# Performance work log

Hardware: AMD Instinct MI355X
Metric: run time of the kernel (lower is better)

The kernel has to match this reference:

```python
import jax, jax.numpy as jnp
import numpy as np

N, E, D = 100000, 1600000, 64
L = 3          # num_layers
EPS = 1e-5     # LayerNorm eps


def setup_inputs() -> dict:
    key = jax.random.key(0)
    ks = jax.random.split(key, 8)
    s = 0.05
    return {
        "x": jax.random.normal(ks[0], (N, D), jnp.float32),
        "edge_src": jax.random.randint(ks[1], (E,), 0, N, jnp.int32),
        "edge_dst": jax.random.randint(ks[2], (E,), 0, N, jnp.int32),
        # SAGEConv: lin_l (on aggregated neighbors, with bias), lin_r (root, no bias)
        "w_l": (jax.random.normal(ks[3], (L, D, D)) * s).astype(jnp.float32),
        "b_l": jnp.zeros((L, D), jnp.float32),
        "w_r": (jax.random.normal(ks[4], (L, D, D)) * s).astype(jnp.float32),
        # LayerNorm affine params per layer
        "gamma": jnp.ones((L, D), jnp.float32),
        "beta": jnp.zeros((L, D), jnp.float32),
        # residual projection (layer 0 only; Identity afterwards)
        "w_res": (jax.random.normal(ks[5], (D, D)) * s).astype(jnp.float32),
        "b_res": jnp.zeros((D,), jnp.float32),
        # final fc
        "w_fc": (jax.random.normal(ks[6], (D, D)) * s).astype(jnp.float32),
        "b_fc": jnp.zeros((D,), jnp.float32),
    }


def _layer_norm(h, g, b):
    mu = jnp.mean(h, axis=-1, keepdims=True)
    var = jnp.var(h, axis=-1, keepdims=True)
    return (h - mu) * jax.lax.rsqrt(var + EPS) * g + b


def reference(x, edge_src, edge_dst, w_l, b_l, w_r, gamma, beta, w_res, b_res, w_fc, b_fc):
    n = x.shape[0]
    # in-degree for mean aggregation (nodes with no in-edges get 0 aggregate)
    deg = jax.ops.segment_sum(jnp.ones(edge_dst.shape, x.dtype), edge_dst, num_segments=n)
    inv_deg = jnp.where(deg > 0, 1.0 / jnp.maximum(deg, 1.0), 0.0)[:, None]  # [N,1]
    for i in range(L):
        residual = x @ w_res + b_res if i == 0 else x
        # SAGEConv mean aggregation: gather source feats, scatter-sum at dst, divide by degree
        agg = jax.ops.segment_sum(x[edge_src], edge_dst, num_segments=n) * inv_deg  # [N,D]
        h = agg @ w_l[i] + b_l[i] + x @ w_r[i]
        h = jax.nn.relu(_layer_norm(h, gamma[i], beta[i]))
        # dropout is inactive in eval mode
        x = h + residual
    return x @ w_fc + b_fc
```

## Files before the change

### kernel.cpp

```cpp
#include <hip/hip_runtime.h>

typedef unsigned short u16;
typedef __bf16 bf16x8 __attribute__((ext_vector_type(8)));
typedef float f32x4 __attribute__((ext_vector_type(4)));

#define D 64
#define LPITCH 136
#define CHUNKS 1024
#define BSHIFT 9
#define CAPB 10240
#define CCAP 1280

__device__ __forceinline__ float b2f(u16 u) {
    unsigned v = ((unsigned)u) << 16;
    float f;
    __builtin_memcpy(&f, &v, 4);
    return f;
}
__device__ __forceinline__ float u2f_lo(unsigned u) {
    unsigned v = u << 16;
    float f;
    __builtin_memcpy(&f, &v, 4);
    return f;
}
__device__ __forceinline__ float u2f_hi(unsigned u) {
    unsigned v = u & 0xFFFF0000u;
    float f;
    __builtin_memcpy(&f, &v, 4);
    return f;
}
__device__ __forceinline__ u16 f2b(float f) {
    unsigned u;
    __builtin_memcpy(&u, &f, 4);
    u = u + 0x7FFFu + ((u >> 16) & 1u);
    return (u16)(u >> 16);
}
__device__ __forceinline__ bf16x8 ld_frag(const u16* p) {
    union { uint4 u; bf16x8 b; } cv;
    cv.u = *(const uint4*)p;
    return cv.b;
}

__global__ __launch_bounds__(256) void binAB_kernel(
    const int* __restrict__ src, const int* __restrict__ dst, int E,
    int* __restrict__ gcnt,
    int* __restrict__ staging,
    const float* __restrict__ xf, u16* __restrict__ xb, int total4,
    const float* __restrict__ wl, const float* __restrict__ wr,
    const float* __restrict__ wres, const float* __restrict__ wfc,
    u16* __restrict__ WtL, u16* __restrict__ WresT, u16* __restrict__ WfcT,
    int nbuck, int eper) {
    __shared__ int hist[512];
    __shared__ int cur[512];
    int t = threadIdx.x;
    int c = blockIdx.x;
    int gid = c * 256 + t;
    int gstr = CHUNKS * 256;
    int beg = c * eper, end = min(beg + eper, E);

    hist[t] = 0;
    hist[t + 256] = 0;
    __syncthreads();
    for (int i = beg + t; i < end; i += 256)
        atomicAdd(&hist[dst[i] >> BSHIFT], 1);

    for (int i = gid; i < total4; i += gstr) {
        float4 v = *(const float4*)(xf + i * 4);
        ushort4 o;
        o.x = f2b(v.x); o.y = f2b(v.y); o.z = f2b(v.z); o.w = f2b(v.w);
        *(ushort4*)(xb + i * 4) = o;
    }
    for (int idx = gid; idx < 3 * 64 * 128; idx += gstr) {
        int l = idx >> 13;
        int rem = idx & 8191;
        int n = rem >> 7;
        int k = rem & 127;
        float v = (k < 64) ? wl[l * 4096 + k * 64 + n] : wr[l * 4096 + (k - 64) * 64 + n];
        WtL[idx] = f2b(v);
    }
    for (int idx = gid; idx < 4096; idx += gstr) {
        int n = idx >> 6, k = idx & 63;
        WresT[idx] = f2b(wres[k * 64 + n]);
        WfcT[idx] = f2b(wfc[k * 64 + n]);
    }
    __syncthreads();

    for (int b = t; b < nbuck; b += 256) {
        int cnt = hist[b];
        int base = 0;
        if (cnt > 0) base = atomicAdd(&gcnt[b], cnt);
        cur[b] = b * CAPB + base;
    }
    __syncthreads();

    const int mask = (1 << BSHIFT) - 1;
    int capg = CAPB;
    for (int i = beg + t; i < end; i += 256) {
        int d = dst[i];
        int b = d >> BSHIFT;
        int p = atomicAdd(&cur[b], 1);
        if (p < b * CAPB + capg)
            staging[p] = src[i] | ((d & mask) << 17);
    }
}

__global__ __launch_bounds__(256) void binC_kernel(const int* __restrict__ staging,
                                                   const int* __restrict__ T,
                                                   int* __restrict__ row_ptr,
                                                   float* __restrict__ inv_deg,
                                                   int* __restrict__ col, int N, int nbuck) {
    __shared__ int cnt[512];
    __shared__ int lrp[512];
    __shared__ int sm[256];
    __shared__ int span[2];
    int b = blockIdx.x;
    int t = threadIdx.x;
    int v = (t < nbuck) ? min(T[t], CAPB) : 0;
    sm[t] = v;
    __syncthreads();
    for (int off = 1; off < 256; off <<= 1) {
        int u = (t >= off) ? sm[t - off] : 0;
        __syncthreads();
        sm[t] += u;
        __syncthreads();
    }
    if (t == b) { span[0] = sm[t] - v; span[1] = sm[t]; }
    if (b == 0 && t == 255) row_ptr[N] = sm[255];
    cnt[t] = 0;
    cnt[t + 256] = 0;
    __syncthreads();
    int sbeg = span[0];
    int scount = span[1] - span[0];
    int pbeg = b * CAPB;
    int node0 = b << BSHIFT;
    int nn = min(1 << BSHIFT, N - node0);
    for (int i = t; i < scount; i += 256)
        atomicAdd(&cnt[staging[pbeg + i] >> 17], 1);
    __syncthreads();
    int c0 = cnt[2 * t], c1 = cnt[2 * t + 1];
    sm[t] = c0 + c1;
    __syncthreads();
    for (int off = 1; off < 256; off <<= 1) {
        int u = (t >= off) ? sm[t - off] : 0;
        __syncthreads();
        sm[t] += u;
        __syncthreads();
    }
    int excl = sm[t] - c0 - c1;
    lrp[2 * t] = excl;
    lrp[2 * t + 1] = excl + c0;
    __syncthreads();
    for (int i = t; i < nn; i += 256) {
        row_ptr[node0 + i] = sbeg + lrp[i];
        int dd = cnt[i];
        inv_deg[node0 + i] = dd > 0 ? 1.0f / (float)dd : 0.0f;
    }
    __syncthreads();
    for (int i = t; i < scount; i += 256) {
        int word = staging[pbeg + i];
        int ld = word >> 17;
        int k = atomicSub(&cnt[ld], 1) - 1;
        col[sbeg + lrp[ld] + k] = word & 0x1FFFF;
    }
}

__global__ __launch_bounds__(256, 4) void layer_kernel(const u16* __restrict__ xb_in,
                                                       const int* __restrict__ row_ptr,
                                                       const int* __restrict__ col,
                                                       const float* __restrict__ inv_deg,
                                                       const u16* __restrict__ Wt,
                                                       const float* __restrict__ bl,
                                                       const float* __restrict__ gam,
                                                       const float* __restrict__ bet,
                                                       const u16* __restrict__ WresT,
                                                       const float* __restrict__ bres,
                                                       const u16* __restrict__ WfcT,
                                                       const float* __restrict__ bfc,
                                                       u16* __restrict__ xb_out,
                                                       float* __restrict__ fout,
                                                       int N, int layer0, int final_) {
    __shared__ __align__(16) u16 sA[64 * LPITCH];
    __shared__ __align__(16) u16 sB[64 * LPITCH];
    __shared__ int lcol[CCAP];
    __shared__ int rp[65];
    __shared__ float ideg[64];
    int tid = threadIdx.x;
    int base = blockIdx.x * 64;
    int lane = tid & 63;
    int w = tid >> 6;

#pragma unroll
    for (int i = 0; i < 4; i++) {
        int idx = i * 256 + tid;
        int r = idx >> 4, c = idx & 15;
        *(uint4*)&sB[r * LPITCH + c * 8] = *(const uint4*)(Wt + idx * 8);
    }
#pragma unroll
    for (int i = 0; i < 2; i++) {
        int idx = i * 256 + tid;
        int r = idx >> 3, c = idx & 7;
        int node = base + r;
        uint4 v = make_uint4(0, 0, 0, 0);
        if (node < N) v = *(const uint4*)(xb_in + node * D + c * 8);
        *(uint4*)&sA[r * LPITCH + 64 + c * 8] = v;
    }
    if (tid < 65) rp[tid] = row_ptr[min(base + tid, N)];
    if (tid < 64) ideg[tid] = (base + tid < N) ? inv_deg[base + tid] : 0.f;
    __syncthreads();

    int e0 = rp[0];
    int tileE = rp[64] - e0;
    bool fits = tileE <= CCAP;
    if (fits) {
        for (int i = tid; i < tileE; i += 256) lcol[i] = col[e0 + i];
    }
    __syncthreads();

    int slot = lane >> 3;
    int chunk = lane & 7;
    auto run_gather = [&](auto LD) {
#pragma unroll
        for (int r = 0; r < 2; r++) {
            int node_l = w * 16 + r * 8 + slot;
            float a0 = 0, a1 = 0, a2 = 0, a3 = 0, a4 = 0, a5 = 0, a6 = 0, a7 = 0;
            int e = rp[node_l], end = rp[node_l + 1];
#define ACC(v)                                          \
    a0 += u2f_lo(v.x); a1 += u2f_hi(v.x);               \
    a2 += u2f_lo(v.y); a3 += u2f_hi(v.y);               \
    a4 += u2f_lo(v.z); a5 += u2f_hi(v.z);               \
    a6 += u2f_lo(v.w); a7 += u2f_hi(v.w);
            for (; e + 7 < end; e += 8) {
                int s0 = LD(e),     s1 = LD(e + 1), s2 = LD(e + 2), s3 = LD(e + 3);
                int s4 = LD(e + 4), s5 = LD(e + 5), s6 = LD(e + 6), s7 = LD(e + 7);
                uint4 v0 = *(const uint4*)(xb_in + s0 * D + chunk * 8);
                uint4 v1 = *(const uint4*)(xb_in + s1 * D + chunk * 8);
                uint4 v2 = *(const uint4*)(xb_in + s2 * D + chunk * 8);
                uint4 v3 = *(const uint4*)(xb_in + s3 * D + chunk * 8);
                uint4 v4 = *(const uint4*)(xb_in + s4 * D + chunk * 8);
                uint4 v5 = *(const uint4*)(xb_in + s5 * D + chunk * 8);
                uint4 v6 = *(const uint4*)(xb_in + s6 * D + chunk * 8);
                uint4 v7 = *(const uint4*)(xb_in + s7 * D + chunk * 8);
                ACC(v0) ACC(v1) ACC(v2) ACC(v3)
                ACC(v4) ACC(v5) ACC(v6) ACC(v7)
            }
            if (e + 3 < end) {
                int s0 = LD(e), s1 = LD(e + 1), s2 = LD(e + 2), s3 = LD(e + 3);
                uint4 v0 = *(const uint4*)(xb_in + s0 * D + chunk * 8);
                uint4 v1 = *(const uint4*)(xb_in + s1 * D + chunk * 8);
                uint4 v2 = *(const uint4*)(xb_in + s2 * D + chunk * 8);
                uint4 v3 = *(const uint4*)(xb_in + s3 * D + chunk * 8);
                ACC(v0) ACC(v1) ACC(v2) ACC(v3)
                e += 4;
            }
            if (e + 1 < end) {
                int s0 = LD(e), s1 = LD(e + 1);
                uint4 v0 = *(const uint4*)(xb_in + s0 * D + chunk * 8);
                uint4 v1 = *(const uint4*)(xb_in + s1 * D + chunk * 8);
                ACC(v0) ACC(v1)
                e += 2;
            }
            if (e < end) {
                int s0 = LD(e);
                uint4 v0 = *(const uint4*)(xb_in + s0 * D + chunk * 8);
                ACC(v0)
            }
#undef ACC
            float m = ideg[node_l];
            uint4 o;
            o.x = (unsigned)f2b(a0 * m) | ((unsigned)f2b(a1 * m) << 16);
            o.y = (unsigned)f2b(a2 * m) | ((unsigned)f2b(a3 * m) << 16);
            o.z = (unsigned)f2b(a4 * m) | ((unsigned)f2b(a5 * m) << 16);
            o.w = (unsigned)f2b(a6 * m) | ((unsigned)f2b(a7 * m) << 16);
            *(uint4*)&sA[node_l * LPITCH + chunk * 8] = o;
        }
    };
    if (fits) run_gather([&](int e) { return lcol[e - e0]; });
    else      run_gather([&](int e) { return col[e]; });
    __syncthreads();

    int q = lane >> 4;
    int ln = lane & 15;
    f32x4 acc[4] = {{0, 0, 0, 0}, {0, 0, 0, 0}, {0, 0, 0, 0}, {0, 0, 0, 0}};
    f32x4 accr[4] = {{0, 0, 0, 0}, {0, 0, 0, 0}, {0, 0, 0, 0}, {0, 0, 0, 0}};
    const u16* aRow = &sA[(w * 16 + ln) * LPITCH];

#pragma unroll
    for (int c = 0; c < 4; c++) {
        bf16x8 a = ld_frag(&aRow[c * 32 + q * 8]);
#pragma unroll
        for (int t = 0; t < 4; t++) {
            bf16x8 b = ld_frag(&sB[(t * 16 + ln) * LPITCH + c * 32 + q * 8]);
            acc[t] = __builtin_amdgcn_mfma_f32_16x16x32_bf16(a, b, acc[t], 0, 0, 0);
        }
    }
    if (layer0) {
#pragma unroll
        for (int c = 0; c < 2; c++) {
            bf16x8 a = ld_frag(&aRow[64 + c * 32 + q * 8]);
#pragma unroll
            for (int t = 0; t < 4; t++) {
                bf16x8 b = ld_frag(WresT + (t * 16 + ln) * 64 + c * 32 + q * 8);
                accr[t] = __builtin_amdgcn_mfma_f32_16x16x32_bf16(a, b, accr[t], 0, 0, 0);
            }
        }
    }

    float bcol[4], gcol[4], btcol[4], brcol[4];
#pragma unroll
    for (int t = 0; t < 4; t++) {
        int colI = t * 16 + ln;
        bcol[t] = bl[colI];
        gcol[t] = gam[colI];
        btcol[t] = bet[colI];
        brcol[t] = layer0 ? bres[colI] : 0.f;
    }
#pragma unroll
    for (int t = 0; t < 4; t++)
#pragma unroll
        for (int r = 0; r < 4; r++) acc[t][r] += bcol[t];

    float ps[4], pq[4];
#pragma unroll
    for (int r = 0; r < 4; r++) {
        float s = 0, s2 = 0;
#pragma unroll
        for (int t = 0; t < 4; t++) { float h = acc[t][r]; s += h; s2 += h * h; }
        ps[r] = s; pq[r] = s2;
    }
    for (int off = 1; off < 16; off <<= 1) {
#pragma unroll
        for (int r = 0; r < 4; r++) {
            ps[r] += __shfl_xor(ps[r], off, 64);
            pq[r] += __shfl_xor(pq[r], off, 64);
        }
    }
#pragma unroll
    for (int r = 0; r < 4; r++) {
        int nb = w * 16 + q * 4 + r;
        float mu = ps[r] * (1.f / 64.f);
        float var = pq[r] * (1.f / 64.f) - mu * mu;
        var = var < 0.f ? 0.f : var;
        float rstd = rsqrtf(var + 1e-5f);
#pragma unroll
        for (int t = 0; t < 4; t++) {
            int colI = t * 16 + ln;
            float hn = (acc[t][r] - mu) * rstd * gcol[t] + btcol[t];
            hn = hn > 0.f ? hn : 0.f;
            float res = layer0 ? (accr[t][r] + brcol[t])
                               : b2f(sA[nb * LPITCH + 64 + colI]);
            sA[nb * LPITCH + colI] = f2b(hn + res);
        }
    }

    if (final_) {
        f32x4 accf[4] = {{0, 0, 0, 0}, {0, 0, 0, 0}, {0, 0, 0, 0}, {0, 0, 0, 0}};
#pragma unroll
        for (int c = 0; c < 2; c++) {
            bf16x8 a = ld_frag(&aRow[c * 32 + q * 8]);
#pragma unroll
            for (int t = 0; t < 4; t++) {
                bf16x8 b = ld_frag(WfcT + (t * 16 + ln) * 64 + c * 32 + q * 8);
                accf[t] = __builtin_amdgcn_mfma_f32_16x16x32_bf16(a, b, accf[t], 0, 0, 0);
            }
        }
        __syncthreads();
        float* fB = (float*)sB;
#pragma unroll
        for (int r = 0; r < 4; r++) {
            int nb = w * 16 + q * 4 + r;
#pragma unroll
            for (int t = 0; t < 4; t++) {
                int colI = t * 16 + ln;
                fB[nb * 68 + colI] = accf[t][r] + bfc[colI];
            }
        }
        __syncthreads();
#pragma unroll
        for (int i = 0; i < 4; i++) {
            int idx = i * 256 + tid;
            int row = idx >> 4, cc = idx & 15;
            int node = base + row;
            if (node < N)
                *(float4*)(fout + node * D + cc * 4) = *(const float4*)&fB[row * 68 + cc * 4];
        }
    } else {
#pragma unroll
        for (int i = 0; i < 2; i++) {
            int idx = i * 64 + lane;
            int row = w * 16 + (idx >> 3);
            int ch = idx & 7;
            int node = base + row;
            if (node < N)
                *(uint4*)(xb_out + node * D + ch * 8) = *(const uint4*)&sA[row * LPITCH + ch * 8];
        }
    }
}

extern "C" void kernel_launch(void* const* d_in, const int* in_sizes, int n_in,
                              void* d_out, int out_size, void* d_ws, size_t ws_size,
                              hipStream_t stream) {
    const float* x_in = (const float*)d_in[0];
    const int* e_src = (const int*)d_in[1];
    const int* e_dst = (const int*)d_in[2];
    const float* w_l = (const float*)d_in[3];
    const float* b_l = (const float*)d_in[4];
    const float* w_r = (const float*)d_in[5];
    const float* gam = (const float*)d_in[6];
    const float* bet = (const float*)d_in[7];
    const float* w_res = (const float*)d_in[8];
    const float* b_res = (const float*)d_in[9];
    const float* w_fc = (const float*)d_in[10];
    const float* b_fc = (const float*)d_in[11];
    float* out = (float*)d_out;

    const int N = in_sizes[0] / D;
    const int E = in_sizes[1];
    const int nbuck = ((N - 1) >> BSHIFT) + 1;
    const int eper = (E + CHUNKS - 1) / CHUNKS;

    size_t o = 0;
    auto carve = [&](size_t bytes) {
        size_t cur = o;
        o += (bytes + 255) & ~(size_t)255;
        return (char*)d_ws + cur;
    };
    int* row_ptr = (int*)carve((size_t)(N + 1) * 4);
    float* inv_deg = (float*)carve((size_t)N * 4);
    int* colA = (int*)carve((size_t)E * 4);
    int* staging = (int*)carve((size_t)nbuck * CAPB * 4);
    int* gcnt = (int*)carve((size_t)nbuck * 4);
    u16* WtL = (u16*)carve(3 * 64 * 128 * 2);
    u16* WresT = (u16*)carve(64 * 64 * 2);
    u16* WfcT = (u16*)carve(64 * 64 * 2);
    u16* xbA = (u16*)carve((size_t)N * D * 2);
    u16* xbB = (u16*)carve((size_t)N * D * 2);

    hipMemsetAsync(gcnt, 0, (size_t)nbuck * 4, stream);
    binAB_kernel<<<CHUNKS, 256, 0, stream>>>(e_src, e_dst, E, gcnt, staging,
                                             x_in, xbA, N * D / 4,
                                             w_l, w_r, w_res, w_fc, WtL, WresT, WfcT,
                                             nbuck, eper);
    binC_kernel<<<nbuck, 256, 0, stream>>>(staging, gcnt, row_ptr, inv_deg, colA,
                                           N, nbuck);

    int gridT = (N + 63) / 64;

    layer_kernel<<<gridT, 256, 0, stream>>>(xbA, row_ptr, colA, inv_deg, WtL,
                                            b_l, gam, bet, WresT, b_res,
                                            WfcT, b_fc, xbB, out, N, 1, 0);
    layer_kernel<<<gridT, 256, 0, stream>>>(xbB, row_ptr, colA, inv_deg, WtL + 8192,
                                            b_l + 64, gam + 64, bet + 64, WresT, b_res,
                                            WfcT, b_fc, xbA, out, N, 0, 0);
    layer_kernel<<<gridT, 256, 0, stream>>>(xbA, row_ptr, colA, inv_deg, WtL + 16384,
                                            b_l + 128, gam + 128, bet + 128, WresT, b_res,
                                            WfcT, b_fc, xbB, out, N, 0, 1);
}
```

Before: 276.0 us.

## Drop shared weight tile in layer kernel and shrink binning buckets to 256 nodes

The layer kernel no longer stages the concatenated weight matrix in shared memory. MFMA B fragments are read directly from global/L2, and the final-FC staging buffer reuses sA. The aim is lower LDS use, allowing 6 blocks per CU instead of 4, at the cost of repeated global weight loads. Binning also drops to 256-node buckets with more chunks and a smaller per-bucket capacity, so the CSR build kernel's scan and count arrays are resized to match.

```diff
diff --git a/kernel.cpp b/kernel.cpp
--- a/kernel.cpp
+++ b/kernel.cpp
@@ -6,9 +6,9 @@
 
 #define D 64
 #define LPITCH 136
-#define CHUNKS 1024
-#define BSHIFT 9
-#define CAPB 10240
+#define CHUNKS 2048
+#define BSHIFT 8
+#define CAPB 4608
 #define CCAP 1280
 
 __device__ __forceinline__ float b2f(u16 u) {
@@ -94,12 +94,11 @@
     __syncthreads();
 
     const int mask = (1 << BSHIFT) - 1;
-    int capg = CAPB;
     for (int i = beg + t; i < end; i += 256) {
         int d = dst[i];
         int b = d >> BSHIFT;
         int p = atomicAdd(&cur[b], 1);
-        if (p < b * CAPB + capg)
+        if (p < (b + 1) * CAPB)
             staging[p] = src[i] | ((d & mask) << 17);
     }
 }
@@ -109,14 +108,16 @@
                                                    int* __restrict__ row_ptr,
                                                    float* __restrict__ inv_deg,
                                                    int* __restrict__ col, int N, int nbuck) {
-    __shared__ int cnt[512];
-    __shared__ int lrp[512];
+    __shared__ int cnt[256];
+    __shared__ int lrp[256];
     __shared__ int sm[256];
     __shared__ int span[2];
     int b = blockIdx.x;
     int t = threadIdx.x;
-    int v = (t < nbuck) ? min(T[t], CAPB) : 0;
-    sm[t] = v;
+    int v0 = (2 * t < nbuck) ? min(T[2 * t], CAPB) : 0;
+    int v1 = (2 * t + 1 < nbuck) ? min(T[2 * t + 1], CAPB) : 0;
+    int s = v0 + v1;
+    sm[t] = s;
     __syncthreads();
     for (int off = 1; off < 256; off <<= 1) {
         int u = (t >= off) ? sm[t - off] : 0;
@@ -124,10 +125,11 @@
         sm[t] += u;
         __syncthreads();
     }
-    if (t == b) { span[0] = sm[t] - v; span[1] = sm[t]; }
+    int base0 = sm[t] - s;
+    if (2 * t == b)     { span[0] = base0;      span[1] = base0 + v0; }
+    if (2 * t + 1 == b) { span[0] = base0 + v0; span[1] = base0 + v0 + v1; }
     if (b == 0 && t == 255) row_ptr[N] = sm[255];
     cnt[t] = 0;
-    cnt[t + 256] = 0;
     __syncthreads();
     int sbeg = span[0];
     int scount = span[1] - span[0];
@@ -137,8 +139,8 @@
     for (int i = t; i < scount; i += 256)
         atomicAdd(&cnt[staging[pbeg + i] >> 17], 1);
     __syncthreads();
-    int c0 = cnt[2 * t], c1 = cnt[2 * t + 1];
-    sm[t] = c0 + c1;
+    int c0 = cnt[t];
+    sm[t] = c0;
     __syncthreads();
     for (int off = 1; off < 256; off <<= 1) {
         int u = (t >= off) ? sm[t - off] : 0;
@@ -146,14 +148,11 @@
         sm[t] += u;
         __syncthreads();
     }
-    int excl = sm[t] - c0 - c1;
-    lrp[2 * t] = excl;
-    lrp[2 * t + 1] = excl + c0;
-    __syncthreads();
-    for (int i = t; i < nn; i += 256) {
-        row_ptr[node0 + i] = sbeg + lrp[i];
-        int dd = cnt[i];
-        inv_deg[node0 + i] = dd > 0 ? 1.0f / (float)dd : 0.0f;
+    lrp[t] = sm[t] - c0;
+    __syncthreads();
+    if (t < nn) {
+        row_ptr[node0 + t] = sbeg + lrp[t];
+        inv_deg[node0 + t] = c0 > 0 ? 1.0f / (float)c0 : 0.0f;
     }
     __syncthreads();
     for (int i = t; i < scount; i += 256) {
@@ -164,7 +163,7 @@
     }
 }
 
-__global__ __launch_bounds__(256, 4) void layer_kernel(const u16* __restrict__ xb_in,
+__global__ __launch_bounds__(256, 6) void layer_kernel(const u16* __restrict__ xb_in,
                                                        const int* __restrict__ row_ptr,
                                                        const int* __restrict__ col,
                                                        const float* __restrict__ inv_deg,
@@ -180,7 +179,6 @@
                                                        float* __restrict__ fout,
                                                        int N, int layer0, int final_) {
     __shared__ __align__(16) u16 sA[64 * LPITCH];
-    __shared__ __align__(16) u16 sB[64 * LPITCH];
     __shared__ int lcol[CCAP];
     __shared__ int rp[65];
     __shared__ float ideg[64];
@@ -189,12 +187,6 @@
     int lane = tid & 63;
     int w = tid >> 6;
 
-#pragma unroll
-    for (int i = 0; i < 4; i++) {
-        int idx = i * 256 + tid;
-        int r = idx >> 4, c = idx & 15;
-        *(uint4*)&sB[r * LPITCH + c * 8] = *(const uint4*)(Wt + idx * 8);
-    }
 #pragma unroll
     for (int i = 0; i < 2; i++) {
         int idx = i * 256 + tid;
@@ -289,7 +281,7 @@
         bf16x8 a = ld_frag(&aRow[c * 32 + q * 8]);
 #pragma unroll
         for (int t = 0; t < 4; t++) {
-            bf16x8 b = ld_frag(&sB[(t * 16 + ln) * LPITCH + c * 32 + q * 8]);
+            bf16x8 b = ld_frag(Wt + (t * 16 + ln) * 128 + c * 32 + q * 8);
             acc[t] = __builtin_amdgcn_mfma_f32_16x16x32_bf16(a, b, acc[t], 0, 0, 0);
         }
     }
@@ -364,7 +356,7 @@
             }
         }
         __syncthreads();
-        float* fB = (float*)sB;
+        float* fB = (float*)sA;
 #pragma unroll
         for (int r = 0; r < 4; r++) {
             int nb = w * 16 + q * 4 + r;
```

Measured after the change: 347.9 us. 1.26x slower.
